# Performance work log

Hardware: AMD Instinct MI355X
Metric: run time of the kernel (lower is better)

## Reference

```python
import jax, jax.numpy as jnp
import numpy as np

N, E, D, G, L = 50000, 400000, 64, 256, 4
VA, VB = 64, 8   # atom / bond feature vocab sizes
NUM_ATOM_FEATS, NUM_BOND_FEATS = 9, 3
MSG_EPS = 1e-7   # GENConv message epsilon
LN_EPS = 1e-5


def layernorm(x, g, b):
    mu = x.mean(-1, keepdims=True)
    var = x.var(-1, keepdims=True)
    return (x - mu) * jax.lax.rsqrt(var + LN_EPS) * g + b


def genconv(h, edge_emb, src, dst, W, b):
    # GENConv (aggr='softmax', t=1, mlp_layers=1):
    # msg = relu(x_j + e) + eps; per-dst per-feature softmax-weighted sum; mlp(x + m)
    msg = jax.nn.relu(h[src] + edge_emb) + MSG_EPS          # [E, D]
    mmax = jax.ops.segment_max(msg, dst, num_segments=N)    # [N, D]
    mmax = jnp.where(jnp.isfinite(mmax), mmax, 0.0)         # nodes with no in-edges
    ex = jnp.exp(msg - mmax[dst])
    denom = jax.ops.segment_sum(ex, dst, num_segments=N)
    alpha = ex / jnp.maximum(denom[dst], 1e-16)
    m = jax.ops.segment_sum(alpha * msg, dst, num_segments=N)  # [N, D]
    return (h + m) @ W + b


def setup_inputs():
    key = jax.random.key(0)
    ks = jax.random.split(key, 10)
    x = jax.random.randint(ks[0], (N, NUM_ATOM_FEATS), 0, VA)
    edge_index = jax.random.randint(ks[1], (2, E), 0, N)
    edge_attr = jax.random.randint(ks[2], (E, NUM_BOND_FEATS), 0, VB)
    batch = jnp.sort(jax.random.randint(ks[3], (N,), 0, G))
    s = 0.02
    w = 1.0 / np.sqrt(D).astype(np.float32)
    atom_emb = jax.random.normal(ks[4], (NUM_ATOM_FEATS, VA, D), jnp.float32) * s
    bond_emb = jax.random.normal(ks[5], (NUM_BOND_FEATS, VB, D), jnp.float32) * s
    gcn_W = jax.random.normal(ks[6], (L, D, D), jnp.float32) * w
    gcn_b = jnp.zeros((L, D), jnp.float32)
    norm_g = jnp.ones((L, D), jnp.float32)
    norm_b = jnp.zeros((L, D), jnp.float32)
    vn_emb = jnp.zeros((1, D), jnp.float32)  # constant-init virtualnode embedding
    vn_W1 = jax.random.normal(ks[7], (L - 1, D, D), jnp.float32) * w
    vn_b1 = jnp.zeros((L - 1, D), jnp.float32)
    vn_g1 = jnp.ones((L - 1, D), jnp.float32)
    vn_be1 = jnp.zeros((L - 1, D), jnp.float32)
    vn_W2 = jax.random.normal(ks[8], (L - 1, D, D), jnp.float32) * w
    vn_b2 = jnp.zeros((L - 1, D), jnp.float32)
    vn_g2 = jnp.ones((L - 1, D), jnp.float32)
    vn_be2 = jnp.zeros((L - 1, D), jnp.float32)
    return dict(x=x, edge_index=edge_index, edge_attr=edge_attr, batch=batch,
                atom_emb=atom_emb, bond_emb=bond_emb, gcn_W=gcn_W, gcn_b=gcn_b,
                norm_g=norm_g, norm_b=norm_b, vn_emb=vn_emb,
                vn_W1=vn_W1, vn_b1=vn_b1, vn_g1=vn_g1, vn_be1=vn_be1,
                vn_W2=vn_W2, vn_b2=vn_b2, vn_g2=vn_g2, vn_be2=vn_be2)


def reference(x, edge_index, edge_attr, batch, atom_emb, bond_emb, gcn_W, gcn_b,
              norm_g, norm_b, vn_emb, vn_W1, vn_b1, vn_g1, vn_be1,
              vn_W2, vn_b2, vn_g2, vn_be2):
    src, dst = edge_index[0], edge_index[1]
    # AtomEncoder / BondEncoder: sum of per-feature embedding lookups
    h = atom_emb[jnp.arange(NUM_ATOM_FEATS)[None, :], x].sum(1)          # [N, D]
    edge_emb = bond_emb[jnp.arange(NUM_BOND_FEATS)[None, :], edge_attr].sum(1)  # [E, D]
    vn = jnp.broadcast_to(vn_emb[0], (G, D))
    h = h + vn[batch]
    # block == 'res+' (eval mode: dropout is identity)
    h = genconv(h, edge_emb, src, dst, gcn_W[0], gcn_b[0])
    for l in range(1, L):
        h2 = jax.nn.relu(layernorm(h, norm_g[l - 1], norm_b[l - 1]))
        vt = jax.ops.segment_sum(h2, batch, num_segments=G) + vn         # global_add_pool
        vt = jax.nn.relu(layernorm(vt @ vn_W1[l - 1] + vn_b1[l - 1], vn_g1[l - 1], vn_be1[l - 1]))
        vn = jax.nn.relu(layernorm(vt @ vn_W2[l - 1] + vn_b2[l - 1], vn_g2[l - 1], vn_be2[l - 1]))
        h2 = h2 + vn[batch]
        h = genconv(h2, edge_emb, src, dst, gcn_W[l], gcn_b[l]) + h
    return layernorm(h, norm_g[L - 1], norm_b[L - 1])
```

## Files before the change

### kernel.cpp

```cpp
#include <hip/hip_runtime.h>
#include <hip/hip_bf16.h>

typedef __hip_bfloat16 bf16;

#define GNUM 256
#define LN_EPS 1e-5f
#define MSG_EPS 1e-7f

typedef float f4v __attribute__((ext_vector_type(4)));
typedef short s8v __attribute__((ext_vector_type(8)));
typedef __bf16 b8v __attribute__((ext_vector_type(8)));

template <typename V>
__device__ auto mfma_bf16_(V a, V b, f4v c, int)
    -> decltype(__builtin_amdgcn_mfma_f32_16x16x32_bf16(a, b, c, 0, 0, 0)) {
  return __builtin_amdgcn_mfma_f32_16x16x32_bf16(a, b, c, 0, 0, 0);
}
template <typename V>
__device__ f4v mfma_bf16_(V a, V b, f4v c, long) {
  return __builtin_amdgcn_mfma_f32_16x16x32_bf16(__builtin_bit_cast(s8v, a),
                                                 __builtin_bit_cast(s8v, b), c, 0, 0, 0);
}
__device__ __forceinline__ f4v mfma16(uint4 a, uint4 b, f4v c){
  return mfma_bf16_(__builtin_bit_cast(b8v, a), __builtin_bit_cast(b8v, b), c, 0);
}

__device__ __forceinline__ float bu2f(unsigned short u){
  unsigned v = ((unsigned)u) << 16; return __builtin_bit_cast(float, v);
}
__device__ __forceinline__ unsigned short f2bu(float f){
  unsigned u = __builtin_bit_cast(unsigned, f);
  return (unsigned short)((u + 0x7FFFu + ((u >> 16) & 1u)) >> 16);
}

__device__ __forceinline__ float wave_sum64(float v){
  #pragma unroll
  for (int off = 32; off > 0; off >>= 1) v += __shfl_xor(v, off, 64);
  return v;
}

struct Params15 {
  const void* src[15];
  int n[15];
  int off[15];
};


__global__ __launch_bounds__(256) void k_front(
    Params15 P, int* __restrict__ flag, float* __restrict__ par,
    int* __restrict__ counts, float* __restrict__ vt, int nvt,
    const int* __restrict__ x, const int* __restrict__ batch,
    unsigned short* __restrict__ Wf, int* __restrict__ goffs,
    unsigned short* __restrict__ b0, int n){
  __shared__ int isf_sh;
  int tid = threadIdx.x, bid = blockIdx.x;
  if (tid < 64){
    const unsigned short* u = (const unsigned short*)P.src[0];
    int bad = 0;
    for (int k = tid; k < 256; k += 64){
      unsigned short v = u[2*k];
      if (((v >> 7) & 0xFFu) >= 137u) bad = 1;
    }
    unsigned long long m = __ballot(bad);
    if (tid == 0) isf_sh = (m != 0ull) ? 1 : 0;
  }
  __syncthreads();
  bool isf = (isf_sh != 0);

  if (bid < 128){
    if (bid == 0 && tid == 0) *flag = isf ? 1 : 0;
    int stride = 128*256;
    int gid = bid*256 + tid;
    for (int a = 0; a < 15; ++a){
      int nn = P.n[a];
      float* d = par + P.off[a];
      if (isf){
        const float* s = (const float*)P.src[a];
        for (int i = gid; i < nn; i += stride) d[i] = s[i];
      } else {
        const bf16* s = (const bf16*)P.src[a];
        for (int i = gid; i < nn; i += stride) d[i] = __bfloat162float(s[i]);
      }
    }
    for (int i = gid; i < n; i += stride) counts[i] = 0;
    for (int i = gid; i < nvt; i += stride) vt[i] = 0.f;
  } else if (bid < 192){
    int t = (bid - 128)*256 + tid;
    int j = t & 7, lane = (t >> 3) & 63, nt = (t >> 9) & 3, kt = (t >> 11) & 1, l = t >> 12;
    int k = kt*32 + (lane >> 4)*8 + j;
    int c = nt*16 + (lane & 15);
    int src = l*4096 + k*64 + c;
    if (isf) Wf[t] = f2bu(((const float*)P.src[2])[src]);
    else     Wf[t] = ((const unsigned short*)P.src[2])[src];
  } else if (bid < 194){
    int g = (bid - 192)*256 + tid;
    if (g > GNUM) return;
    if (g == GNUM){ goffs[GNUM] = n; return; }
    int lo = 0, hi = n;
    while (lo < hi){ int mid = (lo+hi)>>1; if (batch[mid] < g) lo = mid+1; else hi = mid; }
    goffs[g] = lo;
  } else {
    int t = (bid - 194) * 256 + tid;
    int i = t >> 6, j = t & 63;
    if (i >= n) return;
    float acc;
    if (isf){
      const float* ae = (const float*)P.src[0];
      acc = ((const float*)P.src[6])[j];
      #pragma unroll
      for (int f = 0; f < 9; ++f){
        int idx = x[i*9 + f];
        acc += ae[(f*64 + idx)*64 + j];
      }
    } else {
      const unsigned short* ae = (const unsigned short*)P.src[0];
      acc = bu2f(((const unsigned short*)P.src[6])[j]);
      #pragma unroll
      for (int f = 0; f < 9; ++f){
        int idx = x[i*9 + f];
        acc += bu2f(ae[(f*64 + idx)*64 + j]);
      }
    }
    b0[t] = f2bu(acc);
  }
}

__global__ void k_count(const int* __restrict__ dst, int* __restrict__ counts, int E){
  int e = blockIdx.x*256 + threadIdx.x;
  if (e < E) atomicAdd(counts + dst[e], 1);
}

__global__ __launch_bounds__(256) void k_scan1(const int* __restrict__ counts,
                                               int* __restrict__ offs,
                                               int* __restrict__ btot, int n){
  __shared__ int wsum[4];
  int tid = threadIdx.x, w = tid >> 6, lane = tid & 63;
  int i = blockIdx.x*256 + tid;
  int v = (i < n) ? counts[i] : 0;
  int incl = v;
  #pragma unroll
  for (int off = 1; off < 64; off <<= 1){
    int t = __shfl_up(incl, off, 64);
    if (lane >= off) incl += t;
  }
  if (lane == 63) wsum[w] = incl;
  __syncthreads();
  int woff = 0;
  for (int k = 0; k < w; ++k) woff += wsum[k];
  int tot = incl + woff;
  if (i < n) offs[i+1] = tot;
  if (tid == 255) btot[blockIdx.x] = tot;
}

__global__ __launch_bounds__(256) void k_scan2(const int* __restrict__ btot,
                                               int* __restrict__ bexc, int nb){
  __shared__ int wsum[4];
  __shared__ int carry_sh;
  int tid = threadIdx.x, w = tid >> 6, lane = tid & 63;
  if (tid == 0) carry_sh = 0;
  __syncthreads();
  for (int base = 0; base < nb; base += 256){
    int i = base + tid;
    int v = (i < nb) ? btot[i] : 0;
    int incl = v;
    #pragma unroll
    for (int off = 1; off < 64; off <<= 1){
      int t = __shfl_up(incl, off, 64);
      if (lane >= off) incl += t;
    }
    if (lane == 63) wsum[w] = incl;
    __syncthreads();
    int carry = carry_sh;
    int woff = 0;
    for (int k = 0; k < w; ++k) woff += wsum[k];
    if (i < nb) bexc[i] = carry + woff + incl - v;
    __syncthreads();
    if (tid == 0) carry_sh = carry + wsum[0] + wsum[1] + wsum[2] + wsum[3];
    __syncthreads();
  }
}

__global__ void k_scan3(int* __restrict__ offs, int* __restrict__ cursor,
                        const int* __restrict__ bexc, int n){
  int i = blockIdx.x*256 + threadIdx.x;
  if (i == 0){ offs[0] = 0; cursor[0] = 0; }
  if (i < n){
    int v = offs[i+1] + bexc[blockIdx.x];
    offs[i+1] = v;
    if (i+1 < n) cursor[i+1] = v;
  }
}

__global__ void k_scatter(const int* __restrict__ src, const int* __restrict__ dst,
                          const int* __restrict__ ea, int* __restrict__ cursor,
                          int* __restrict__ payload, int E){
  int e = blockIdx.x*256 + threadIdx.x;
  if (e >= E) return;
  int d = dst[e];
  int pos = atomicAdd(cursor + d, 1);
  payload[pos] = (src[e] & 0xFFFF) | (ea[e*3] << 16) | (ea[e*3+1] << 19) | (ea[e*3+2] << 22);
}

__global__ __launch_bounds__(256) void k_layer(
    const unsigned short* __restrict__ b0, const int* __restrict__ offs,
    const int* __restrict__ payload, const float* __restrict__ bond,
    const unsigned short* __restrict__ Wf, const float* __restrict__ bias,
    const int* __restrict__ batch, float* __restrict__ vt,
    unsigned short* __restrict__ hres, float2* __restrict__ rowstat,
    void* __restrict__ finalout, const float* __restrict__ ng,
    const float* __restrict__ nb, const int* __restrict__ flag,
    int use_res, int mode, int n){
  __shared__ float Bs[1536];
  __shared__ __align__(16) unsigned short T[16][72];
  __shared__ float PS1[4][16], PS2[4][16];
  __shared__ int batch_lds[16];
  int tid = threadIdx.x;
  int v0 = blockIdx.x * 16;
  for (int idx = tid; idx < 1536; idx += 256) Bs[idx] = bond[idx];
  if (tid < 16){ int rw = v0 + tid; batch_lds[tid] = (rw < n) ? batch[rw] : -1; }
  __syncthreads();
  int w = tid >> 6, j = tid & 63;
  int vb = v0 + w*4;

  int oidx = vb + (j < 5 ? j : 4);
  if (oidx > n) oidx = n;
  int o5 = offs[oidx];

  for (int r = 0; r < 4; ++r){
    int v = vb + r;
    float tv = 0.f;
    if (v < n){
      int e0 = __builtin_amdgcn_readfirstlane(__shfl(o5, r, 64));
      int e1 = __builtin_amdgcn_readfirstlane(__shfl(o5, r + 1, 64));
      float own = bu2f(b0[((unsigned)v << 6) + j]);
      tv = own;
      if (e1 > e0){
        float den = 0.f, num = 0.f;
        int rem0 = e1 - e0;
        if (rem0 <= 8){
          int pu[8]; float hv[8];
          #pragma unroll
          for (int u = 0; u < 8; ++u){
            int ei = (u < rem0) ? e0 + u : e0;
            pu[u] = payload[ei];
          }
          #pragma unroll
          for (int u = 0; u < 8; ++u)
            hv[u] = bu2f(b0[((unsigned)(pu[u] & 0xFFFF) << 6) + j]);
          if (rem0 >= 8){
            #pragma unroll
            for (int u = 0; u < 8; ++u){
              int p = pu[u];
              float eev = Bs[((p >> 16) & 7)*64 + j]
                        + Bs[(8 + ((p >> 19) & 7))*64 + j]
                        + Bs[(16 + ((p >> 22) & 7))*64 + j];
              float mm = fmaxf(hv[u] + eev, 0.f) + MSG_EPS;
              float ex = __expf(mm);
              den += ex;
              num = fmaf(ex, mm, num);
            }
          } else {
            #pragma unroll
            for (int u = 0; u < 8; ++u){
              if (u < rem0){
                int p = pu[u];
                float eev = Bs[((p >> 16) & 7)*64 + j]
                          + Bs[(8 + ((p >> 19) & 7))*64 + j]
                          + Bs[(16 + ((p >> 22) & 7))*64 + j];
                float mm = fmaxf(hv[u] + eev, 0.f) + MSG_EPS;
                float ex = __expf(mm);
                den += ex;
                num = fmaf(ex, mm, num);
              }
            }
          }
        } else {
          int pu[16]; float hv[16];
          #pragma unroll
          for (int u = 0; u < 16; ++u){
            int ei = (u < rem0) ? e0 + u : e0;
            pu[u] = payload[ei];
          }
          #pragma unroll
          for (int u = 0; u < 16; ++u)
            hv[u] = bu2f(b0[((unsigned)(pu[u] & 0xFFFF) << 6) + j]);
          if (rem0 >= 16){
            #pragma unroll
            for (int u = 0; u < 16; ++u){
              int p = pu[u];
              float eev = Bs[((p >> 16) & 7)*64 + j]
                        + Bs[(8 + ((p >> 19) & 7))*64 + j]
                        + Bs[(16 + ((p >> 22) & 7))*64 + j];
              float mm = fmaxf(hv[u] + eev, 0.f) + MSG_EPS;
              float ex = __expf(mm);
              den += ex;
              num = fmaf(ex, mm, num);
            }
          } else {
            #pragma unroll
            for (int u = 0; u < 16; ++u){
              if (u < rem0){
                int p = pu[u];
                float eev = Bs[((p >> 16) & 7)*64 + j]
                          + Bs[(8 + ((p >> 19) & 7))*64 + j]
                          + Bs[(16 + ((p >> 22) & 7))*64 + j];
                float mm = fmaxf(hv[u] + eev, 0.f) + MSG_EPS;
                float ex = __expf(mm);
                den += ex;
                num = fmaf(ex, mm, num);
              }
            }
          }
          for (int e = e0 + 16; e < e1; e += 8){
            int rem = e1 - e;
            int pu8[8]; float hv8[8];
            #pragma unroll
            for (int u = 0; u < 8; ++u){
              int ei = (u < rem) ? e + u : e0;
              pu8[u] = payload[ei];
            }
            #pragma unroll
            for (int u = 0; u < 8; ++u)
              hv8[u] = bu2f(b0[((unsigned)(pu8[u] & 0xFFFF) << 6) + j]);
            #pragma unroll
            for (int u = 0; u < 8; ++u){
              if (u < rem){
                int p = pu8[u];
                float eev = Bs[((p >> 16) & 7)*64 + j]
                          + Bs[(8 + ((p >> 19) & 7))*64 + j]
                          + Bs[(16 + ((p >> 22) & 7))*64 + j];
                float mm = fmaxf(hv8[u] + eev, 0.f) + MSG_EPS;
                float ex = __expf(mm);
                den += ex;
                num = fmaf(ex, mm, num);
              }
            }
          }
        }
        tv = own + num / fmaxf(den, 1e-16f);
      }
    }
    T[w*4 + r][j] = f2bu(tv);
  }
  __syncthreads();

  int ct = w;
  int quad = j >> 4, lm = j & 15;
  const uint4* Wfv = (const uint4*)Wf;
  uint4 B0 = Wfv[(size_t)(0*4 + ct)*64 + j];
  uint4 B1 = Wfv[(size_t)(1*4 + ct)*64 + j];
  uint4 A0 = *(const uint4*)&T[lm][8*quad];
  uint4 A1 = *(const uint4*)&T[lm][32 + 8*quad];
  f4v acc = (f4v){0.f,0.f,0.f,0.f};
  acc = mfma16(A0, B0, acc);
  acc = mfma16(A1, B1, acc);

  int col = ct*16 + lm;
  float bv = bias[col];
  float s1[4], s2[4];
  #pragma unroll
  for (int reg = 0; reg < 4; ++reg){
    int row = v0 + quad*4 + reg;
    float val = acc[reg] + bv;
    if (use_res && row < n) val += bu2f(hres[((unsigned)row << 6) + col]);
    acc[reg] = val;
    s1[reg] = val;
    s2[reg] = val*val;
  }
  #pragma unroll
  for (int reg = 0; reg < 4; ++reg){
    #pragma unroll
    for (int m = 1; m < 16; m <<= 1){
      s1[reg] += __shfl_xor(s1[reg], m, 64);
      s2[reg] += __shfl_xor(s2[reg], m, 64);
    }
  }
  if (lm == 0){
    #pragma unroll
    for (int reg = 0; reg < 4; ++reg){
      int rl = quad*4 + reg;
      PS1[ct][rl] = s1[reg];
      PS2[ct][rl] = s2[reg];
    }
  }
  __syncthreads();

  if (mode == 0){
    float* H2 = Bs;
    #pragma unroll
    for (int reg = 0; reg < 4; ++reg){
      int rl = quad*4 + reg;
      int row = v0 + rl;
      if (row >= n) continue;
      hres[((size_t)row << 6) + col] = f2bu(acc[reg]);
      float t1 = PS1[0][rl] + PS1[1][rl] + PS1[2][rl] + PS1[3][rl];
      float t2 = PS2[0][rl] + PS2[1][rl] + PS2[2][rl] + PS2[3][rl];
      float mu = t1 * (1.f/64.f);
      float var = fmaxf(t2 * (1.f/64.f) - mu*mu, 0.f);
      float rstd = rsqrtf(var + LN_EPS);
      if (ct == 0 && lm == 0) rowstat[row] = make_float2(mu, rstd);
      H2[rl*65 + col] = fmaxf((acc[reg] - mu) * rstd * ng[col] + nb[col], 0.f);
    }
    __syncthreads();
    float a = 0.f; int gc = -1;
    #pragma unroll
    for (int r = 0; r < 4; ++r){
      int rl = w*4 + r;
      int g = batch_lds[rl];
      if (g >= 0){
        if (g != gc){
          if (gc >= 0) atomicAdd(&vt[(unsigned)gc*64 + j], a);
          gc = g; a = 0.f;
        }
        a += H2[rl*65 + j];
      }
    }
    if (gc >= 0) atomicAdd(&vt[(unsigned)gc*64 + j], a);
    return;
  }

  bool isf = (*flag != 0);
  #pragma unroll
  for (int reg = 0; reg < 4; ++reg){
    int rl = quad*4 + reg;
    int row = v0 + rl;
    if (row >= n) continue;
    float t1 = PS1[0][rl] + PS1[1][rl] + PS1[2][rl] + PS1[3][rl];
    float t2 = PS2[0][rl] + PS2[1][rl] + PS2[2][rl] + PS2[3][rl];
    float mu = t1 * (1.f/64.f);
    float var = fmaxf(t2 * (1.f/64.f) - mu*mu, 0.f);
    float rstd = rsqrtf(var + LN_EPS);
    float y = (acc[reg] - mu) * rstd * ng[col] + nb[col];
    size_t o = ((size_t)row << 6) + col;
    if (isf) ((float*)finalout)[o] = y;
    else     ((bf16*)finalout)[o]  = __float2bfloat16(y);
  }
}

__global__ __launch_bounds__(512) void k_vn(
    const unsigned short* __restrict__ hres, const float2* __restrict__ rowstat,
    float* __restrict__ vt, const int* __restrict__ goffs,
    const float* __restrict__ vn_emb, float* __restrict__ vn,
    unsigned short* __restrict__ b0,
    const float* __restrict__ ng, const float* __restrict__ nbb,
    const float* __restrict__ W1, const float* __restrict__ b1,
    const float* __restrict__ g1, const float* __restrict__ be1,
    const float* __restrict__ W2, const float* __restrict__ b2,
    const float* __restrict__ g2, const float* __restrict__ be2,
    int first){
  __shared__ float Ws[4096];
  __shared__ float rowbuf[64];
  __shared__ float vnew[64];
  int tid = threadIdx.x, w = tid >> 6, j = tid & 63, g = blockIdx.x;
  float ngj = ng[j], nbj = nbb[j];
  for (int idx = tid; idx < 4096; idx += 512) Ws[idx] = W1[idx];
  int r0 = goffs[g], r1 = goffs[g+1];
  if (tid < 64){
    float s = vt[(unsigned)g*64 + j]
            + (first ? vn_emb[j] : vn[(unsigned)g*64 + j]);
    vt[(unsigned)g*64 + j] = 0.f;
    rowbuf[j] = s;
  }
  __syncthreads();
  float y = 0.f;
  if (tid < 64){
    float acc = b1[j];
    #pragma unroll
    for (int k = 0; k < 64; ++k) acc = fmaf(rowbuf[k], Ws[k*64 + j], acc);
    float mu = wave_sum64(acc) * (1.f/64.f);
    float d = acc - mu;
    float var = wave_sum64(d*d) * (1.f/64.f);
    y = fmaxf(d * rsqrtf(var + LN_EPS) * g1[j] + be1[j], 0.f);
  }
  __syncthreads();
  for (int idx = tid; idx < 4096; idx += 512) Ws[idx] = W2[idx];
  if (tid < 64) rowbuf[j] = y;
  __syncthreads();
  if (tid < 64){
    float acc = b2[j];
    #pragma unroll
    for (int k = 0; k < 64; ++k) acc = fmaf(rowbuf[k], Ws[k*64 + j], acc);
    float mu = wave_sum64(acc) * (1.f/64.f);
    float d = acc - mu;
    float var = wave_sum64(d*d) * (1.f/64.f);
    float v2 = fmaxf(d * rsqrtf(var + LN_EPS) * g2[j] + be2[j], 0.f);
    vn[(unsigned)g*64 + j] = v2;
    vnew[j] = v2;
  }
  __syncthreads();
  float vj = vnew[j];
  for (int i = r0 + w; i < r1; i += 8){
    float xv = bu2f(hres[((unsigned)i << 6) + j]);
    float2 st = rowstat[i];
    float h2 = fmaxf((xv - st.x) * st.y * ngj + nbj, 0.f);
    b0[((unsigned)i << 6) + j] = f2bu(h2 + vj);
  }
}

extern "C" void kernel_launch(void* const* d_in, const int* in_sizes, int n_in,
                              void* d_out, int out_size, void* d_ws, size_t ws_size,
                              hipStream_t stream){
  const int* x          = (const int*)d_in[0];
  const int* edge_index = (const int*)d_in[1];
  const int* edge_attr  = (const int*)d_in[2];
  const int* batch      = (const int*)d_in[3];

  const int N = in_sizes[3];
  const int E = in_sizes[2] / 3;
  const int L = 4;

  const int P_ATOM = 0, P_BOND = 36864, P_GW = 38400, P_GB = 54784,
            P_NG = 55040, P_NB = 55296, P_VNE = 55552, P_W1 = 55616,
            P_B1 = 67904, P_G1 = 68096, P_BE1 = 68288, P_W2 = 68480,
            P_B2 = 80768, P_G2 = 80960, P_BE2 = 81152, P_END = 81344;

  char* ws = (char*)d_ws;
  size_t off = 0;
  auto alloc = [&](size_t bytes)->char*{
    char* p = ws + off; off += (bytes + 255) & ~(size_t)255; return p;
  };
  int*    flag   = (int*)alloc(256);
  float*  par    = (float*)alloc((size_t)P_END * 4);
  unsigned short* Wf  = (unsigned short*)alloc(16384 * 2);
  unsigned short* b0  = (unsigned short*)alloc((size_t)N*64*2);
  unsigned short* hres= (unsigned short*)alloc((size_t)N*64*2);
  float2* rowstat= (float2*)alloc((size_t)N*8);
  float*  vt     = (float*)alloc((size_t)GNUM*64*4);
  int*    counts = (int*)alloc((size_t)N*4);
  int*    offs   = (int*)alloc((size_t)(N+1)*4);
  int*    cursor = (int*)alloc((size_t)N*4);
  int*    btot   = (int*)alloc(1024);
  int*    bexc   = (int*)alloc(1024);
  int*    payload= (int*)alloc((size_t)E*4);
  int*    goffs  = (int*)alloc((size_t)(GNUM+1)*4);
  float*  vn     = (float*)alloc((size_t)GNUM*64*4);
  (void)ws_size; (void)n_in; (void)out_size;

  Params15 P;
  const int poffs[15] = {P_ATOM,P_BOND,P_GW,P_GB,P_NG,P_NB,P_VNE,P_W1,P_B1,P_G1,P_BE1,P_W2,P_B2,P_G2,P_BE2};
  for (int a = 0; a < 15; ++a){ P.src[a] = d_in[4+a]; P.n[a] = in_sizes[4+a]; P.off[a] = poffs[a]; }

  int nodeGrid = (N*64 + 255) / 256;
  int nScanB   = (N + 255) / 256;
  int eGrid    = (E + 255) / 256;
  const int* srcp = edge_index;
  const int* dstp = edge_index + E;

  k_front<<<194 + nodeGrid, 256, 0, stream>>>(P, flag, par, counts, vt, GNUM*64,
                                              x, batch, Wf, goffs, b0, N);
  k_count<<<eGrid, 256, 0, stream>>>(dstp, counts, E);
  k_scan1<<<nScanB, 256, 0, stream>>>(counts, offs, btot, N);
  k_scan2<<<1, 256, 0, stream>>>(btot, bexc, nScanB);
  k_scan3<<<nScanB, 256, 0, stream>>>(offs, cursor, bexc, N);
  k_scatter<<<eGrid, 256, 0, stream>>>(srcp, dstp, edge_attr, cursor, payload, E);

  int layerGrid = (N + 15) / 16;
  for (int l = 0; l < L; ++l){
    if (l > 0){
      k_vn<<<GNUM, 512, 0, stream>>>(hres, rowstat, vt, goffs, par + P_VNE, vn, b0,
                                     par + P_NG + (l-1)*64, par + P_NB + (l-1)*64,
                                     par + P_W1 + (l-1)*4096, par + P_B1 + (l-1)*64,
                                     par + P_G1 + (l-1)*64, par + P_BE1 + (l-1)*64,
                                     par + P_W2 + (l-1)*4096, par + P_B2 + (l-1)*64,
                                     par + P_G2 + (l-1)*64, par + P_BE2 + (l-1)*64,
                                     l == 1 ? 1 : 0);
    }
    int mode = (l == L-1) ? 1 : 0;
    k_layer<<<layerGrid, 256, 0, stream>>>(b0, offs, payload, par + P_BOND,
                                           Wf + (size_t)l*4096, par + P_GB + l*64,
                                           batch, vt, hres, rowstat, d_out,
                                           par + P_NG + l*64, par + P_NB + l*64,
                                           flag, l > 0 ? 1 : 0, mode, N);
  }
}
```

Baseline: 332.4 us.

## Fuse edge counting into front kernel and merge scan fixup with scatter

Moves the in-degree atomic count into extra blocks of the front kernel, with counts zeroed by a memset beforehand. The scan now writes block-local exclusive cursors directly, and the final offset fixup is fused with the edge scatter, which adds the block prefix to each atomic position. This cuts two kernel launches and the barriers between them from the CSR build, at the cost of an extra memset and a slightly more involved position computation.

```diff
diff --git a/kernel.cpp b/kernel.cpp
--- a/kernel.cpp
+++ b/kernel.cpp
@@ -50,8 +50,9 @@
     Params15 P, int* __restrict__ flag, float* __restrict__ par,
     int* __restrict__ counts, float* __restrict__ vt, int nvt,
     const int* __restrict__ x, const int* __restrict__ batch,
+    const int* __restrict__ dstp,
     unsigned short* __restrict__ Wf, int* __restrict__ goffs,
-    unsigned short* __restrict__ b0, int n){
+    unsigned short* __restrict__ b0, int n, int E, int eGrid){
   __shared__ int isf_sh;
   int tid = threadIdx.x, bid = blockIdx.x;
   if (tid < 64){
@@ -82,7 +83,6 @@
         for (int i = gid; i < nn; i += stride) d[i] = __bfloat162float(s[i]);
       }
     }
-    for (int i = gid; i < n; i += stride) counts[i] = 0;
     for (int i = gid; i < nvt; i += stride) vt[i] = 0.f;
   } else if (bid < 192){
     int t = (bid - 128)*256 + tid;
@@ -99,8 +99,11 @@
     int lo = 0, hi = n;
     while (lo < hi){ int mid = (lo+hi)>>1; if (batch[mid] < g) lo = mid+1; else hi = mid; }
     goffs[g] = lo;
+  } else if (bid < 194 + eGrid){
+    int e = (bid - 194)*256 + tid;
+    if (e < E) atomicAdd(counts + dstp[e], 1);
   } else {
-    int t = (bid - 194) * 256 + tid;
+    int t = (bid - 194 - eGrid) * 256 + tid;
     int i = t >> 6, j = t & 63;
     if (i >= n) return;
     float acc;
@@ -125,13 +128,9 @@
   }
 }
 
-__global__ void k_count(const int* __restrict__ dst, int* __restrict__ counts, int E){
-  int e = blockIdx.x*256 + threadIdx.x;
-  if (e < E) atomicAdd(counts + dst[e], 1);
-}
-
 __global__ __launch_bounds__(256) void k_scan1(const int* __restrict__ counts,
                                                int* __restrict__ offs,
+                                               int* __restrict__ cursor,
                                                int* __restrict__ btot, int n){
   __shared__ int wsum[4];
   int tid = threadIdx.x, w = tid >> 6, lane = tid & 63;
@@ -148,7 +147,10 @@
   int woff = 0;
   for (int k = 0; k < w; ++k) woff += wsum[k];
   int tot = incl + woff;
-  if (i < n) offs[i+1] = tot;
+  if (i < n){
+    offs[i+1] = tot;
+    cursor[i] = tot - v;
+  }
   if (tid == 255) btot[blockIdx.x] = tot;
 }
 
@@ -180,25 +182,22 @@
   }
 }
 
-__global__ void k_scan3(int* __restrict__ offs, int* __restrict__ cursor,
-                        const int* __restrict__ bexc, int n){
-  int i = blockIdx.x*256 + threadIdx.x;
-  if (i == 0){ offs[0] = 0; cursor[0] = 0; }
-  if (i < n){
-    int v = offs[i+1] + bexc[blockIdx.x];
-    offs[i+1] = v;
-    if (i+1 < n) cursor[i+1] = v;
-  }
-}
-
-__global__ void k_scatter(const int* __restrict__ src, const int* __restrict__ dst,
-                          const int* __restrict__ ea, int* __restrict__ cursor,
-                          int* __restrict__ payload, int E){
-  int e = blockIdx.x*256 + threadIdx.x;
-  if (e >= E) return;
-  int d = dst[e];
-  int pos = atomicAdd(cursor + d, 1);
-  payload[pos] = (src[e] & 0xFFFF) | (ea[e*3] << 16) | (ea[e*3+1] << 19) | (ea[e*3+2] << 22);
+__global__ void k_scatfin(const int* __restrict__ src, const int* __restrict__ dst,
+                          const int* __restrict__ ea, int* __restrict__ offs,
+                          int* __restrict__ cursor, const int* __restrict__ bexc,
+                          int* __restrict__ payload, int n, int E, int nScanB){
+  int bid = blockIdx.x, tid = threadIdx.x;
+  if (bid < nScanB){
+    int i = bid*256 + tid;
+    if (i == 0) offs[0] = 0;
+    if (i < n) offs[i+1] += bexc[bid];
+  } else {
+    int e = (bid - nScanB)*256 + tid;
+    if (e >= E) return;
+    int d = dst[e];
+    int pos = atomicAdd(cursor + d, 1) + bexc[d >> 8];
+    payload[pos] = (src[e] & 0xFFFF) | (ea[e*3] << 16) | (ea[e*3+1] << 19) | (ea[e*3+2] << 22);
+  }
 }
 
 __global__ __launch_bounds__(256) void k_layer(
@@ -546,13 +545,15 @@
   const int* srcp = edge_index;
   const int* dstp = edge_index + E;
 
-  k_front<<<194 + nodeGrid, 256, 0, stream>>>(P, flag, par, counts, vt, GNUM*64,
-                                              x, batch, Wf, goffs, b0, N);
-  k_count<<<eGrid, 256, 0, stream>>>(dstp, counts, E);
-  k_scan1<<<nScanB, 256, 0, stream>>>(counts, offs, btot, N);
+  hipMemsetAsync(counts, 0, (size_t)N*4, stream);
+  k_front<<<194 + eGrid + nodeGrid, 256, 0, stream>>>(P, flag, par, counts,
+                                                      vt, GNUM*64, x, batch,
+                                                      dstp, Wf, goffs, b0,
+                                                      N, E, eGrid);
+  k_scan1<<<nScanB, 256, 0, stream>>>(counts, offs, cursor, btot, N);
   k_scan2<<<1, 256, 0, stream>>>(btot, bexc, nScanB);
-  k_scan3<<<nScanB, 256, 0, stream>>>(offs, cursor, bexc, N);
-  k_scatter<<<eGrid, 256, 0, stream>>>(srcp, dstp, edge_attr, cursor, payload, E);
+  k_scatfin<<<nScanB + eGrid, 256, 0, stream>>>(srcp, dstp, edge_attr, offs,
+                                                cursor, bexc, payload, N, E, nScanB);
 
   int layerGrid = (N + 15) / 16;
   for (int l = 0; l < L; ++l){
```

Result: no change. 332.6 us, median of 2 (+0.1%).
